# Kernel optimization log

Measured on AMD Instinct MI355X. Metric: run time of the kernel, lower is better.

## Reference

```python
import jax, jax.numpy as jnp
import numpy as np

B, S, D = 4, 1024, 1024
H, DK, DH = 16, 64, 64  # num_heads, key_size, head_size
NEG = 1e12


def setup_inputs() -> dict:
    key = jax.random.key(0)
    ks = jax.random.split(key, 16)
    scale = 0.02
    inp = {
        'q': jax.random.normal(ks[0], (B, S, D), jnp.float32),
        'k': jax.random.normal(ks[1], (B, S, D), jnp.float32),
        'v': jax.random.normal(ks[2], (B, S, D), jnp.float32),
        'v_mask': jax.random.randint(ks[3], (B, S), 0, 2, jnp.int32),
        'q_mask': jax.random.randint(ks[4], (B, S), 0, 2, jnp.int32),
        # causal attention mask (float, 1 = keep)
        'a_mask': jnp.tril(jnp.ones((S, S), jnp.float32))[None, None, :, :],
        'Wq': jax.random.normal(ks[5], (D, H * DK), jnp.float32) * scale,
        'bq': jnp.zeros((H * DK,), jnp.float32),
        'Wk': jax.random.normal(ks[6], (D, H * DK), jnp.float32) * scale,
        'bk': jnp.zeros((H * DK,), jnp.float32),
        'Wv': jax.random.normal(ks[7], (D, H * DH), jnp.float32) * scale,
        'bv': jnp.zeros((H * DH,), jnp.float32),
        'Wo': jax.random.normal(ks[8], (H * DH, H * DH), jnp.float32) * scale,
        'bo': jnp.zeros((H * DH,), jnp.float32),
    }
    return inp


def reference(q, k, v, v_mask, q_mask, a_mask, Wq, bq, Wk, bk, Wv, bv, Wo, bo):
    b, sq, _ = q.shape
    sk = k.shape[1]
    qw = (jnp.einsum('bsd,de->bse', q, Wq) + bq).reshape(b, sq, H, DK)
    kw = (jnp.einsum('bsd,de->bse', k, Wk) + bk).reshape(b, sk, H, DK)
    vw = (jnp.einsum('bsd,de->bse', v, Wv) + bv).reshape(b, sk, H, DH)
    # scores [b, h, sq, sk]
    a = jnp.einsum('bjhd,bkhd->bhjk', qw, kw) / jnp.sqrt(jnp.float32(DK))
    vm = v_mask.astype(jnp.float32)  # [b, sk]
    a = a - (1.0 - vm)[:, None, None, :] * NEG  # sequence_masking mode='add'
    a = a - (1.0 - a_mask) * NEG                # attention mask
    p = jax.nn.softmax(a, axis=-1)
    o = jnp.einsum('bhjk,bkhd->bjhd', p, vw).reshape(b, sq, H * DH)
    o = jnp.einsum('bse,ef->bsf', o, Wo) + bo
    qm = q_mask.astype(jnp.float32)
    o = o * qm[:, :, None]  # sequence_masking mode='mul'
    return o
```

## Files before the change

### kernel.cpp

```cpp
#include <hip/hip_runtime.h>
#include <cstdint>
#include <cstddef>

typedef unsigned short u16;
using short8 = __attribute__((ext_vector_type(8))) short;
using f32x4  = __attribute__((ext_vector_type(4))) float;

constexpr int Sc = 1024;
constexpr float PEN = 60.0f;

__device__ __forceinline__ u16 f2bf(float f) {
  union { float f; uint32_t u; } v; v.f = f;
  return (u16)((v.u + 0x7fffu + ((v.u >> 16) & 1u)) >> 16);
}

__device__ __forceinline__ void gload_lds16(const u16* g, u16* l) {
  __builtin_amdgcn_global_load_lds(
      (const __attribute__((address_space(1))) uint32_t*)g,
      (__attribute__((address_space(3))) uint32_t*)l, 16, 0, 0);
}

__device__ __forceinline__ f32x4 mfma16(short8 a, short8 b, f32x4 c) {
  return __builtin_amdgcn_mfma_f32_16x16x32_bf16(a, b, c, 0, 0, 0);
}

__global__ __launch_bounds__(256) void cvt3(const float* __restrict__ q,
                                            const float* __restrict__ k,
                                            const float* __restrict__ v,
                                            u16* __restrict__ qb,
                                            u16* __restrict__ kb,
                                            u16* __restrict__ vb) {
  const float* src = blockIdx.y == 0 ? q : blockIdx.y == 1 ? k : v;
  u16* dst = blockIdx.y == 0 ? qb : blockIdx.y == 1 ? kb : vb;
  int i = blockIdx.x * 256 + threadIdx.x;
  float4 a = ((const float4*)src)[2 * i];
  float4 b = ((const float4*)src)[2 * i + 1];
  u16 t[8] = {f2bf(a.x), f2bf(a.y), f2bf(a.z), f2bf(a.w),
              f2bf(b.x), f2bf(b.y), f2bf(b.z), f2bf(b.w)};
  ((uint4*)dst)[i] = *(const uint4*)t;
}

__global__ __launch_bounds__(256) void transpose_cvt4(
    const float* __restrict__ W0, const float* __restrict__ W1,
    const float* __restrict__ W2, const float* __restrict__ W3,
    u16* __restrict__ D0, u16* __restrict__ D1, u16* __restrict__ D2,
    u16* __restrict__ D3) {
  const float* W = blockIdx.z == 0 ? W0 : blockIdx.z == 1 ? W1
                 : blockIdx.z == 2 ? W2 : W3;
  u16* WT = blockIdx.z == 0 ? D0 : blockIdx.z == 1 ? D1
          : blockIdx.z == 2 ? D2 : D3;
  __shared__ float t[32][33];
  int bx = blockIdx.x * 32, by = blockIdx.y * 32;
  int tx = threadIdx.x & 31, ty = threadIdx.x >> 5;
  for (int i = 0; i < 32; i += 8)
    t[ty + i][tx] = W[(size_t)(by + ty + i) * 1024 + bx + tx];
  __syncthreads();
  for (int i = 0; i < 32; i += 8)
    WT[(size_t)(bx + ty + i) * 1024 + by + tx] = f2bf(t[tx][ty + i]);
}

__global__ __launch_bounds__(256) void gemm_qkv(
    const u16* __restrict__ qb, const u16* __restrict__ kb,
    const u16* __restrict__ vb, const u16* __restrict__ BT,
    const float* __restrict__ bq, const float* __restrict__ bk,
    const float* __restrict__ bv, u16* __restrict__ QW, u16* __restrict__ KW,
    u16* __restrict__ VTg) {
  const int bid = blockIdx.x;
  const int xcd = bid & 7, local = bid >> 3;
  const int mp = local & 3, nbi = local >> 2;
  const int m0 = (xcd * 4 + mp) * 128, n0 = nbi * 128;
  const int seg = nbi >> 3;
  const u16* A    = seg == 0 ? qb : seg == 1 ? kb : vb;
  const float* bias = seg == 0 ? bq : seg == 1 ? bk : bv;

  __shared__ u16 As[128 * 32];
  __shared__ u16 Bs[128 * 32];

  const int t = threadIdx.x, w = t >> 6, lane = t & 63;
  const int q4 = lane >> 4, lm = lane & 15;
  const int wm = (w >> 1) * 64, wn = (w & 1) * 64;
  const int srow = lane >> 2, p = lane & 3;
  const int cf = q4 ^ ((lm >> 2) & 3);

  f32x4 acc[4][4] = {};

  for (int k0 = 0; k0 < 1024; k0 += 32) {
    __syncthreads();
    for (int j = 0; j < 2; ++j) {
      const int rbase = (w * 2 + j) * 16;
      const int row = rbase + srow;
      const int c = p ^ ((row >> 2) & 3);
      gload_lds16(&A[(size_t)(m0 + row) * 1024 + k0 + c * 8], &As[rbase * 32]);
      gload_lds16(&BT[(size_t)(n0 + row) * 1024 + k0 + c * 8], &Bs[rbase * 32]);
    }
    __syncthreads();
    short8 af[4], bf[4];
    for (int mi = 0; mi < 4; ++mi)
      af[mi] = *(const short8*)&As[(wm + mi * 16 + lm) * 32 + cf * 8];
    for (int ni = 0; ni < 4; ++ni)
      bf[ni] = *(const short8*)&Bs[(wn + ni * 16 + lm) * 32 + cf * 8];
    for (int mi = 0; mi < 4; ++mi)
      for (int ni = 0; ni < 4; ++ni)
        acc[mi][ni] = mfma16(af[mi], bf[ni], acc[mi][ni]);
  }
  if (seg < 2) {
    u16* C = seg == 0 ? QW : KW;
    for (int mi = 0; mi < 4; ++mi)
      for (int ni = 0; ni < 4; ++ni)
        for (int r = 0; r < 4; ++r) {
          int row = m0 + wm + mi * 16 + q4 * 4 + r;
          int col = (n0 + wn + ni * 16 + lm) & 1023;
          C[(size_t)row * 1024 + col] = f2bf(acc[mi][ni][r] + bias[col]);
        }
  } else {
    for (int mi = 0; mi < 4; ++mi)
      for (int ni = 0; ni < 4; ++ni) {
        int row0 = m0 + wm + mi * 16 + q4 * 4;
        int col = (n0 + wn + ni * 16 + lm) & 1023;
        float bv4 = bias[col];
        u16 o4[4];
        for (int r = 0; r < 4; ++r) o4[r] = f2bf(acc[mi][ni][r] + bv4);
        *(uint2*)&VTg[(size_t)col * 4096 + row0] = *(const uint2*)o4;
      }
  }
}

__global__ __launch_bounds__(256) void gemm_out(
    const u16* __restrict__ A, const u16* __restrict__ BT,
    const float* __restrict__ bias, const int* __restrict__ qmask,
    float* __restrict__ Cf) {
  const int bid = blockIdx.x;
  const int xcd = bid & 7, local = bid >> 3;
  const int mp = local & 7, nb = local >> 3;
  const int m0 = (xcd * 8 + mp) * 64, n0 = nb * 128;

  __shared__ u16 As[64 * 32];
  __shared__ u16 Bs[128 * 32];
  const int t = threadIdx.x, w = t >> 6, lane = t & 63;
  const int q4 = lane >> 4, lm = lane & 15;
  const int wm = (w >> 1) * 32, wn = (w & 1) * 64;
  const int srow = lane >> 2, p = lane & 3;
  const int cf = q4 ^ ((lm >> 2) & 3);

  f32x4 acc[2][4] = {};

  for (int k0 = 0; k0 < 1024; k0 += 32) {
    __syncthreads();
    {
      const int row = w * 16 + srow;
      const int c = p ^ ((row >> 2) & 3);
      gload_lds16(&A[(size_t)(m0 + row) * 1024 + k0 + c * 8], &As[w * 512]);
    }
    for (int j = 0; j < 2; ++j) {
      const int rbase = (w * 2 + j) * 16;
      const int row = rbase + srow;
      const int c = p ^ ((row >> 2) & 3);
      gload_lds16(&BT[(size_t)(n0 + row) * 1024 + k0 + c * 8], &Bs[rbase * 32]);
    }
    __syncthreads();
    short8 af[2], bf[4];
    for (int mi = 0; mi < 2; ++mi)
      af[mi] = *(const short8*)&As[(wm + mi * 16 + lm) * 32 + cf * 8];
    for (int ni = 0; ni < 4; ++ni)
      bf[ni] = *(const short8*)&Bs[(wn + ni * 16 + lm) * 32 + cf * 8];
    for (int mi = 0; mi < 2; ++mi)
      for (int ni = 0; ni < 4; ++ni)
        acc[mi][ni] = mfma16(af[mi], bf[ni], acc[mi][ni]);
  }

  for (int mi = 0; mi < 2; ++mi)
    for (int ni = 0; ni < 4; ++ni)
      for (int r = 0; r < 4; ++r) {
        int row = m0 + wm + mi * 16 + q4 * 4 + r;
        int col = n0 + wn + ni * 16 + lm;
        Cf[(size_t)row * 1024 + col] =
            (acc[mi][ni][r] + bias[col]) * (float)qmask[row];
      }
}

__global__ __launch_bounds__(256) void attn(
    const u16* __restrict__ QW, const u16* __restrict__ KW,
    const u16* __restrict__ VTg, const int* __restrict__ vmask,
    u16* __restrict__ O) {
  const int bid = blockIdx.x;
  const int xcd = bid & 7, local = bid >> 3;
  const int pair = xcd * 8 + (local & 7);
  const int b = pair >> 4, h = pair & 15;
  const int bx = local >> 3;
  const int qta = bx, qtb = 15 - bx;
  const int t = threadIdx.x, w = t >> 6, lane = t & 63;
  const int q4 = lane >> 4, lm = lane & 15;

  __shared__ u16 Ks[2][64 * 64];
  __shared__ u16 VTs[2][64 * 64];
  __shared__ u16 P[4][16 * 88];
  __shared__ float penv[1024];
  __shared__ int anyf[2];

  if (t < 2) anyf[t] = 0;
  {
    int4 vm = ((const int4*)(vmask + b * 1024))[t];
    penv[4 * t + 0] = (1.f - (float)vm.x) * PEN;
    penv[4 * t + 1] = (1.f - (float)vm.y) * PEN;
    penv[4 * t + 2] = (1.f - (float)vm.z) * PEN;
    penv[4 * t + 3] = (1.f - (float)vm.w) * PEN;
  }
  __syncthreads();
  {
    int any_a = 0, any_b = 0;
    for (int i = t; i <= qtb * 64; i += 256) {
      int un = (penv[i] == 0.f);
      if (i <= qta * 64) any_a |= un;
      any_b |= un;
    }
    if (any_a) atomicOr(&anyf[0], 1);
    if (any_b) atomicOr(&anyf[1], 1);
  }
  __syncthreads();
  const int extA = !anyf[0], extB = !anyf[1];
  const int kend = (extA || extB) ? 15 : qtb;

  short8 qf[2][2];
  for (int s = 0; s < 2; ++s) {
    int qt = s ? qtb : qta;
    const u16* qp = &QW[(size_t)(b * Sc + qt * 64 + w * 16 + lm) * 1024 + h * 64];
    qf[s][0] = *(const short8*)&qp[q4 * 8];
    qf[s][1] = *(const short8*)&qp[32 + q4 * 8];
    for (int fi = 0; fi < 2; ++fi)
      for (int i = 0; i < 8; ++i) {
        u16 x = (u16)qf[s][fi][i];
        int e = (x >> 7) & 0xff;
        qf[s][fi][i] = (short)(e > 3 ? (u16)(x - 0x180) : (u16)(x & 0x8000));
      }
  }

  float l_run[2][4] = {};
  f32x4 oacc[2][4] = {};

  const int r0 = lane >> 3, pos = lane & 7, ch = pos ^ r0;
  auto stage = [&](int kt, int buf) {
    for (int j = 0; j < 2; ++j) {
      int issue = w * 2 + j;
      int row = issue * 8 + r0;
      gload_lds16(&KW[(size_t)(b * Sc + kt * 64 + row) * 1024 + h * 64 + ch * 8],
                  &Ks[buf][issue * 512]);
      gload_lds16(&VTg[(size_t)(h * 64 + row) * 4096 + b * Sc + kt * 64 + ch * 8],
                  &VTs[buf][issue * 512]);
    }
  };

  auto strip_tile = [&](int s, int kt, int mode, int buf) {
    const int qt = s ? qtb : qta;
    const int qrow0 = qt * 64 + w * 16 + q4 * 4;
    f32x4 sacc[4] = {};
    for (int ni = 0; ni < 4; ++ni) {
      int row = ni * 16 + lm;
      short8 kf0 = *(const short8*)&Ks[buf][row * 64 + ((q4 ^ (lm & 7)) * 8)];
      short8 kf1 = *(const short8*)&Ks[buf][row * 64 + (((4 + q4) ^ (lm & 7)) * 8)];
      sacc[ni] = mfma16(qf[s][0], kf0, sacc[ni]);
      sacc[ni] = mfma16(qf[s][1], kf1, sacc[ni]);
    }
    u16* Pw = &P[w][0];
    for (int ni = 0; ni < 4; ++ni) {
      int key = kt * 64 + ni * 16 + lm;
      float pen = penv[key];
      if (mode == 2) pen += PEN;
      for (int r = 0; r < 4; ++r) {
        float x = sacc[ni][r] - pen;
        if (mode == 1 && key > qrow0 + r) x -= PEN;
        float pv = __expf(x);
        l_run[s][r] += pv;
        Pw[(q4 * 4 + r) * 88 + ni * 16 + lm] = f2bf(pv);
      }
    }
    short8 pf0 = *(const short8*)&Pw[lm * 88 + q4 * 8];
    short8 pf1 = *(const short8*)&Pw[lm * 88 + 32 + q4 * 8];
    for (int ni = 0; ni < 4; ++ni) {
      int row = ni * 16 + lm;
      short8 vf0 = *(const short8*)&VTs[buf][row * 64 + ((q4 ^ (lm & 7)) * 8)];
      short8 vf1 = *(const short8*)&VTs[buf][row * 64 + (((4 + q4) ^ (lm & 7)) * 8)];
      oacc[s][ni] = mfma16(pf0, vf0, oacc[s][ni]);
      oacc[s][ni] = mfma16(pf1, vf1, oacc[s][ni]);
    }
  };

  stage(0, 0);
  int cur = 0;
  for (int kt = 0; kt <= kend; ++kt) {
    __syncthreads();
    if (kt < kend) stage(kt + 1, cur ^ 1);
    if (kt <= qta) strip_tile(0, kt, kt == qta ? 1 : 0, cur);
    else if (extA) strip_tile(0, kt, 2, cur);
    if (kt <= qtb) strip_tile(1, kt, kt == qtb ? 1 : 0, cur);
    else if (extB) strip_tile(1, kt, 2, cur);
    cur ^= 1;
  }

  for (int s = 0; s < 2; ++s) {
    int qt = s ? qtb : qta;
    for (int r = 0; r < 4; ++r) {
      float l = l_run[s][r];
      for (int off = 1; off < 16; off <<= 1) l += __shfl_xor(l, off, 64);
      l_run[s][r] = 1.0f / l;
    }
    for (int ni = 0; ni < 4; ++ni)
      for (int r = 0; r < 4; ++r) {
        int row = b * Sc + qt * 64 + w * 16 + q4 * 4 + r;
        O[(size_t)row * 1024 + h * 64 + ni * 16 + lm] =
            f2bf(oacc[s][ni][r] * l_run[s][r]);
      }
  }
}

extern "C" void kernel_launch(void* const* d_in, const int* in_sizes, int n_in,
                              void* d_out, int out_size, void* d_ws, size_t ws_size,
                              hipStream_t stream) {
  (void)in_sizes; (void)n_in; (void)out_size; (void)ws_size;
  const float* q  = (const float*)d_in[0];
  const float* k  = (const float*)d_in[1];
  const float* v  = (const float*)d_in[2];
  const int* vmask = (const int*)d_in[3];
  const int* qmask = (const int*)d_in[4];
  const float* Wq = (const float*)d_in[6];
  const float* bq = (const float*)d_in[7];
  const float* Wk = (const float*)d_in[8];
  const float* bk = (const float*)d_in[9];
  const float* Wv = (const float*)d_in[10];
  const float* bv = (const float*)d_in[11];
  const float* Wo = (const float*)d_in[12];
  const float* bo = (const float*)d_in[13];

  char* ws = (char*)d_ws;
  u16* WT3 = (u16*)ws;
  u16* WoT = (u16*)(ws + 6291456);
  u16* QW  = (u16*)(ws + 8388608);
  u16* KW  = (u16*)(ws + 16777216);
  u16* VTg = (u16*)(ws + 25165824);
  u16* Oat = (u16*)(ws + 33554432);
  u16* qb = (u16*)d_out;
  u16* kb = (u16*)d_out + 4194304;
  u16* vb = Oat;

  dim3 tb(256);
  transpose_cvt4<<<dim3(32, 32, 4), tb, 0, stream>>>(
      Wq, Wk, Wv, Wo, WT3, WT3 + 1048576, WT3 + 2097152, WoT);
  cvt3<<<dim3(2048, 3), tb, 0, stream>>>(q, k, v, qb, kb, vb);
  gemm_qkv<<<dim3(768), tb, 0, stream>>>(qb, kb, vb, WT3, bq, bk, bv, QW, KW,
                                         VTg);
  attn<<<dim3(512), tb, 0, stream>>>(QW, KW, VTg, vmask, Oat);
  gemm_out<<<dim3(512), tb, 0, stream>>>(Oat, WoT, bo, qmask, (float*)d_out);
}
```

Baseline: 234.6 us.

## Double-buffer LDS staging in QKV and output projection GEMMs

Both projection GEMM kernels now use two LDS buffers per operand. The next K-tile is loaded with global_load_lds while MFMAs run on the current tile, and the loop is unrolled by two, with global pointers precomputed and advanced instead of recomputing addresses each step. The aim is to hide global-load latency behind compute rather than stalling on a load-then-compute barrier pair every iteration. In exchange, LDS use per block doubles, which may lower occupancy, and the overlap relies on the barrier's implicit wait for the async LDS loads.

Measured after the change: 228.0 us. 1.03x faster.

```diff
diff --git a/kernel.cpp b/kernel.cpp
--- a/kernel.cpp
+++ b/kernel.cpp
@@ -73,8 +73,8 @@
   const u16* A    = seg == 0 ? qb : seg == 1 ? kb : vb;
   const float* bias = seg == 0 ? bq : seg == 1 ? bk : bv;
 
-  __shared__ u16 As[128 * 32];
-  __shared__ u16 Bs[128 * 32];
+  __shared__ u16 As0[128 * 32], As1[128 * 32];
+  __shared__ u16 Bs0[128 * 32], Bs1[128 * 32];
 
   const int t = threadIdx.x, w = t >> 6, lane = t & 63;
   const int q4 = lane >> 4, lm = lane & 15;
@@ -82,27 +82,44 @@
   const int srow = lane >> 2, p = lane & 3;
   const int cf = q4 ^ ((lm >> 2) & 3);
 
+  const int rb0 = (w * 2) * 16, rb1 = (w * 2 + 1) * 16;
+  const int rowS0 = rb0 + srow, rowS1 = rb1 + srow;
+  const int c0 = p ^ ((rowS0 >> 2) & 3), c1 = p ^ ((rowS1 >> 2) & 3);
+  const u16* pa0 = &A[(size_t)(m0 + rowS0) * 1024 + c0 * 8];
+  const u16* pa1 = &A[(size_t)(m0 + rowS1) * 1024 + c1 * 8];
+  const u16* pb0 = &BT[(size_t)(n0 + rowS0) * 1024 + c0 * 8];
+  const u16* pb1 = &BT[(size_t)(n0 + rowS1) * 1024 + c1 * 8];
+
   f32x4 acc[4][4] = {};
 
-  for (int k0 = 0; k0 < 1024; k0 += 32) {
-    __syncthreads();
-    for (int j = 0; j < 2; ++j) {
-      const int rbase = (w * 2 + j) * 16;
-      const int row = rbase + srow;
-      const int c = p ^ ((row >> 2) & 3);
-      gload_lds16(&A[(size_t)(m0 + row) * 1024 + k0 + c * 8], &As[rbase * 32]);
-      gload_lds16(&BT[(size_t)(n0 + row) * 1024 + k0 + c * 8], &Bs[rbase * 32]);
-    }
-    __syncthreads();
+  auto stage = [&](u16* as, u16* bs) {
+    gload_lds16(pa0, as + rb0 * 32);
+    gload_lds16(pa1, as + rb1 * 32);
+    gload_lds16(pb0, bs + rb0 * 32);
+    gload_lds16(pb1, bs + rb1 * 32);
+    pa0 += 32; pa1 += 32; pb0 += 32; pb1 += 32;
+  };
+  auto compute = [&](const u16* as, const u16* bs) {
     short8 af[4], bf[4];
     for (int mi = 0; mi < 4; ++mi)
-      af[mi] = *(const short8*)&As[(wm + mi * 16 + lm) * 32 + cf * 8];
+      af[mi] = *(const short8*)&as[(wm + mi * 16 + lm) * 32 + cf * 8];
     for (int ni = 0; ni < 4; ++ni)
-      bf[ni] = *(const short8*)&Bs[(wn + ni * 16 + lm) * 32 + cf * 8];
+      bf[ni] = *(const short8*)&bs[(wn + ni * 16 + lm) * 32 + cf * 8];
     for (int mi = 0; mi < 4; ++mi)
       for (int ni = 0; ni < 4; ++ni)
         acc[mi][ni] = mfma16(af[mi], bf[ni], acc[mi][ni]);
-  }
+  };
+
+  stage(As0, Bs0);
+  for (int it = 0; it < 16; ++it) {
+    __syncthreads();
+    stage(As1, Bs1);
+    compute(As0, Bs0);
+    __syncthreads();
+    if (it < 15) stage(As0, Bs0);
+    compute(As1, Bs1);
+  }
+
   if (seg < 2) {
     u16* C = seg == 0 ? QW : KW;
     for (int mi = 0; mi < 4; ++mi)
@@ -134,38 +151,50 @@
   const int mp = local & 7, nb = local >> 3;
   const int m0 = (xcd * 8 + mp) * 64, n0 = nb * 128;
 
-  __shared__ u16 As[64 * 32];
-  __shared__ u16 Bs[128 * 32];
+  __shared__ u16 As0[64 * 32], As1[64 * 32];
+  __shared__ u16 Bs0[128 * 32], Bs1[128 * 32];
   const int t = threadIdx.x, w = t >> 6, lane = t & 63;
   const int q4 = lane >> 4, lm = lane & 15;
   const int wm = (w >> 1) * 32, wn = (w & 1) * 64;
   const int srow = lane >> 2, p = lane & 3;
   const int cf = q4 ^ ((lm >> 2) & 3);
 
+  const int rowA = w * 16 + srow;
+  const int cA = p ^ ((rowA >> 2) & 3);
+  const int rb0 = (w * 2) * 16, rb1 = (w * 2 + 1) * 16;
+  const int rowS0 = rb0 + srow, rowS1 = rb1 + srow;
+  const int c0 = p ^ ((rowS0 >> 2) & 3), c1 = p ^ ((rowS1 >> 2) & 3);
+  const u16* pa  = &A[(size_t)(m0 + rowA) * 1024 + cA * 8];
+  const u16* pb0 = &BT[(size_t)(n0 + rowS0) * 1024 + c0 * 8];
+  const u16* pb1 = &BT[(size_t)(n0 + rowS1) * 1024 + c1 * 8];
+
   f32x4 acc[2][4] = {};
 
-  for (int k0 = 0; k0 < 1024; k0 += 32) {
-    __syncthreads();
-    {
-      const int row = w * 16 + srow;
-      const int c = p ^ ((row >> 2) & 3);
-      gload_lds16(&A[(size_t)(m0 + row) * 1024 + k0 + c * 8], &As[w * 512]);
-    }
-    for (int j = 0; j < 2; ++j) {
-      const int rbase = (w * 2 + j) * 16;
-      const int row = rbase + srow;
-      const int c = p ^ ((row >> 2) & 3);
-      gload_lds16(&BT[(size_t)(n0 + row) * 1024 + k0 + c * 8], &Bs[rbase * 32]);
-    }
-    __syncthreads();
+  auto stage = [&](u16* as, u16* bs) {
+    gload_lds16(pa, as + w * 512);
+    gload_lds16(pb0, bs + rb0 * 32);
+    gload_lds16(pb1, bs + rb1 * 32);
+    pa += 32; pb0 += 32; pb1 += 32;
+  };
+  auto compute = [&](const u16* as, const u16* bs) {
     short8 af[2], bf[4];
     for (int mi = 0; mi < 2; ++mi)
-      af[mi] = *(const short8*)&As[(wm + mi * 16 + lm) * 32 + cf * 8];
+      af[mi] = *(const short8*)&as[(wm + mi * 16 + lm) * 32 + cf * 8];
     for (int ni = 0; ni < 4; ++ni)
-      bf[ni] = *(const short8*)&Bs[(wn + ni * 16 + lm) * 32 + cf * 8];
+      bf[ni] = *(const short8*)&bs[(wn + ni * 16 + lm) * 32 + cf * 8];
     for (int mi = 0; mi < 2; ++mi)
       for (int ni = 0; ni < 4; ++ni)
         acc[mi][ni] = mfma16(af[mi], bf[ni], acc[mi][ni]);
+  };
+
+  stage(As0, Bs0);
+  for (int it = 0; it < 16; ++it) {
+    __syncthreads();
+    stage(As1, Bs1);
+    compute(As0, Bs0);
+    __syncthreads();
+    if (it < 15) stage(As0, Bs0);
+    compute(As1, Bs1);
   }
 
   for (int mi = 0; mi < 2; ++mi)
```
